# Performance work log

Hardware: AMD Instinct MI355X
Metric: run time of the kernel (lower is better)

## Reference

```python
import jax, jax.numpy as jnp
import numpy as np

H = 512
IN_DIM = 300
NUM_CLASSES = 45
LN_EPS = 1e-5


def _ln(x, g, b):
    m = jnp.mean(x, axis=-1, keepdims=True)
    v = jnp.mean((x - m) ** 2, axis=-1, keepdims=True)
    return (x - m) / jnp.sqrt(v + LN_EPS) * g + b


def _rnn_dir(xemb, Wx, bx, Wh, bh, ln_g, ln_b):
    # xemb: [B, T, H]; Wx/Wh: [3, H, H]; bx/bh: [3, H]; ln_g/ln_b: [3, H]
    B = xemb.shape[0]
    h_init = (jnp.zeros((B, H), xemb.dtype),) * 3

    def step(carry, xt):
        h0, h1, h2 = carry
        h0 = jnp.tanh(_ln(xt @ Wx[0] + bx[0] + h0 @ Wh[0] + bh[0], ln_g[0], ln_b[0]))
        h1 = jnp.tanh(_ln(h0 @ Wx[1] + bx[1] + h1 @ Wh[1] + bh[1], ln_g[1], ln_b[1]))
        h2 = jnp.tanh(_ln(h1 @ Wx[2] + bx[2] + h2 @ Wh[2] + bh[2], ln_g[2], ln_b[2]))
        return (h0, h1, h2), h2

    _, ys = jax.lax.scan(step, h_init, jnp.swapaxes(xemb, 0, 1))  # ys: [T, B, H]
    return jnp.swapaxes(ys, 0, 1)  # [B, T, H]


def setup_inputs() -> dict:
    key = jax.random.key(0)
    ks = jax.random.split(key, 20)
    B, T = 128, 256
    s_in = 1.0 / np.sqrt(IN_DIM)
    s_h = 1.0 / np.sqrt(H)
    inp = {
        "x": jax.random.normal(ks[0], (B, T, IN_DIM), jnp.float32),
        "reverse_x": jax.random.normal(ks[1], (B, T, IN_DIM), jnp.float32),
        "pad_start_index": jax.random.randint(ks[2], (B,), 0, T),
        "max_length": T,
        "W_emb": jax.random.uniform(ks[3], (IN_DIM, H), jnp.float32, -s_in, s_in),
        "b_emb": jax.random.uniform(ks[4], (H,), jnp.float32, -s_in, s_in),
        "Wx_l2r": jax.random.uniform(ks[5], (3, H, H), jnp.float32, -s_h, s_h),
        "bx_l2r": jax.random.uniform(ks[6], (3, H), jnp.float32, -s_h, s_h),
        "Wh_l2r": jax.random.uniform(ks[7], (3, H, H), jnp.float32, -s_h, s_h),
        "bh_l2r": jax.random.uniform(ks[8], (3, H), jnp.float32, -s_h, s_h),
        "Wx_r2l": jax.random.uniform(ks[9], (3, H, H), jnp.float32, -s_h, s_h),
        "bx_r2l": jax.random.uniform(ks[10], (3, H), jnp.float32, -s_h, s_h),
        "Wh_r2l": jax.random.uniform(ks[11], (3, H, H), jnp.float32, -s_h, s_h),
        "bh_r2l": jax.random.uniform(ks[12], (3, H), jnp.float32, -s_h, s_h),
        "ln_g": jnp.ones((3, H), jnp.float32),
        "ln_b": jnp.zeros((3, H), jnp.float32),
        "W_fc": jax.random.uniform(ks[13], (2 * H, NUM_CLASSES), jnp.float32, -1.0 / np.sqrt(2 * H), 1.0 / np.sqrt(2 * H)),
        "b_fc": jax.random.uniform(ks[14], (NUM_CLASSES,), jnp.float32, -1.0 / np.sqrt(2 * H), 1.0 / np.sqrt(2 * H)),
    }
    return inp


def reference(x, reverse_x, pad_start_index, max_length, W_emb, b_emb,
              Wx_l2r, bx_l2r, Wh_l2r, bh_l2r, Wx_r2l, bx_r2l, Wh_r2l, bh_r2l,
              ln_g, ln_b, W_fc, b_fc):
    x = x[:, :max_length]
    reverse_x = reverse_x[:, :max_length]
    x_l2r = x @ W_emb + b_emb           # [B, T, H]
    x_r2l = reverse_x @ W_emb + b_emb
    out_l2r = _rnn_dir(x_l2r, Wx_l2r, bx_l2r, Wh_l2r, bh_l2r, ln_g, ln_b)
    out_r2l = _rnn_dir(x_r2l, Wx_r2l, bx_r2l, Wh_r2l, bh_r2l, ln_g, ln_b)
    T = out_l2r.shape[1]
    j = jnp.arange(T)[None, :]
    p = pad_start_index[:, None]
    idx = jnp.where(j < p, p - j - 1, j)  # [B, T] gather index into r2l time axis
    r2l_g = jnp.take_along_axis(out_r2l, idx[:, :, None], axis=1)
    concat = jnp.concatenate([out_l2r, r2l_g], axis=-1)  # [B, T, 2H]
    logit = concat @ W_fc + b_fc
    return logit.reshape(-1, logit.shape[-1])
```

## Files before the change

kernel.cpp:

```cpp
#include <hip/hip_runtime.h>

#define Bdim 128
#define Tdim 256
#define Hdim 512
#define INdim 300
#define KXdim 320
#define NC 45
#define NTHR 256
#define FPAD 16

typedef _Float16 h16;
typedef __attribute__((ext_vector_type(8))) _Float16 half8;
typedef __attribute__((ext_vector_type(4))) float float4v;
typedef __attribute__((ext_vector_type(2))) float float2v;
typedef __attribute__((ext_vector_type(4))) uint uint4v;
typedef unsigned long long u64;

__device__ __forceinline__ int ld_flag(const int* p) {
    return __hip_atomic_load((int*)p, __ATOMIC_RELAXED, __HIP_MEMORY_SCOPE_AGENT);
}
__device__ __forceinline__ void st_flag_rel(int* p, int v) {
    __hip_atomic_store(p, v, __ATOMIC_RELEASE, __HIP_MEMORY_SCOPE_AGENT);
}

#define WAIT_VM() do { \
    asm volatile("s_waitcnt vmcnt(0)" ::: "memory"); \
    __builtin_amdgcn_sched_barrier(0); \
} while (0)

__device__ __forceinline__ half8 ld16v(const h16* p) {
    half8 r;
    asm volatile("global_load_dwordx4 %0, %1, off sc0 sc1"
                 : "=&v"(r) : "v"(p) : "memory");
    return r;
}
__device__ __forceinline__ float2v ld8vf(const float* p) {
    float2v r;
    asm volatile("global_load_dwordx2 %0, %1, off sc0 sc1"
                 : "=&v"(r) : "v"(p) : "memory");
    return r;
}
__device__ __forceinline__ void st16v(h16* p, half8 v) {
    asm volatile("global_store_dwordx4 %0, %1, off sc0 sc1"
                 :: "v"(p), "v"(v) : "memory");
}
__device__ __forceinline__ void st16vf(float* p, uint4v v) {
    asm volatile("global_store_dwordx4 %0, %1, off sc0 sc1"
                 :: "v"(p), "v"(v) : "memory");
}

__global__ __launch_bounds__(NTHR) void prep1_kernel(
    const float* Wemb, const float* bemb,
    const float* Wx_l2r, const float* bx_l2r, const float* bh_l2r,
    const float* Wx_r2l, const float* bx_r2l, const float* bh_r2l,
    float* W0, float* cb)
{
    int gid = blockIdx.x * NTHR + threadIdx.x;
    const int nW0 = 2 * KXdim * Hdim;
    if (gid < nW0) {
        int dir = gid / (KXdim * Hdim);
        int rem = gid % (KXdim * Hdim);
        int i = rem / Hdim, h = rem % Hdim;
        const float* Wx = dir ? Wx_r2l : Wx_l2r;
        float s = 0.f;
        if (i < INdim) {
            for (int k = 0; k < Hdim; ++k)
                s += Wemb[i * Hdim + k] * Wx[k * Hdim + h];
        }
        W0[gid] = s;
    } else {
        int idx = gid - nW0;
        if (idx < 2 * 3 * Hdim) {
            int dir = idx / (3 * Hdim);
            int l = (idx / Hdim) % 3;
            int h = idx % Hdim;
            const float* Wx = dir ? Wx_r2l : Wx_l2r;
            const float* bx = dir ? bx_r2l : bx_l2r;
            const float* bh = dir ? bh_r2l : bh_l2r;
            float s = bx[l * Hdim + h] + bh[l * Hdim + h];
            if (l == 0) {
                for (int k = 0; k < Hdim; ++k)
                    s += bemb[k] * Wx[k * Hdim + h];
            }
            cb[idx] = s;
        }
    }
}

__global__ __launch_bounds__(NTHR) void pack_W_kernel(
    const float* W0,
    const float* Wx_l2r, const float* Wh_l2r,
    const float* Wx_r2l, const float* Wh_r2l,
    h16* Wfrag)
{
    int e = blockIdx.x * NTHR + threadIdx.x;
    if (e >= 6 * 16 * 32 * 2 * 64 * 8) return;
    int j    = e & 7;
    int lane = (e >> 3) & 63;
    int nt   = (e >> 9) & 1;
    int ks   = (e >> 10) & 31;
    int cs   = (e >> 15) & 15;
    int u    = e >> 19;
    int dir = u / 3, l = u % 3;
    int n  = cs * 32 + nt * 16 + (lane & 15);
    int kk = ks * 32 + ((lane >> 4) * 8) + j;
    float v;
    if (kk < 512) {
        if (l == 0) {
            v = (kk < KXdim) ? W0[(dir * KXdim + kk) * Hdim + n] : 0.f;
        } else {
            const float* Wx = dir ? Wx_r2l : Wx_l2r;
            v = Wx[(l * Hdim + kk) * Hdim + n];
        }
    } else {
        const float* Wh = dir ? Wh_r2l : Wh_l2r;
        v = Wh[(l * Hdim + (kk - 512)) * Hdim + n];
    }
    Wfrag[e] = (h16)v;
}

__global__ __launch_bounds__(NTHR) void pack_W0f_kernel(const float* W0, h16* W0f)
{
    int e = blockIdx.x * NTHR + threadIdx.x;
    if (e >= 2 * 32 * 10 * 64 * 8) return;
    int j    = e & 7;
    int lane = (e >> 3) & 63;
    int rest = e >> 9;
    int ks   = rest % 10;
    rest /= 10;
    int nt   = rest & 31;
    int dir  = rest >> 5;
    int k = ks * 32 + ((lane >> 4) * 8) + j;
    int n = nt * 16 + (lane & 15);
    W0f[e] = (h16)W0[(dir * KXdim + k) * Hdim + n];
}

__global__ __launch_bounds__(NTHR) void zx0_kernel(
    const float* __restrict__ x0, const float* __restrict__ x1,
    const h16* __restrict__ W0f, const float* __restrict__ cb,
    h16* __restrict__ zx0f)
{
    int bx = blockIdx.x;
    int t = bx & 255, mh = (bx >> 8) & 1, dir = bx >> 9;
    const int tid = threadIdx.x;
    __shared__ h16 xl[64 * 328];
    const float* xs = dir ? x1 : x0;
    for (int i = tid; i < 64 * 328; i += NTHR) {
        int r = i / 328, k = i - r * 328;
        int b = mh * 64 + r;
        float v = (k < INdim) ? xs[(b * Tdim + t) * INdim + k] : 0.f;
        xl[i] = (h16)v;
    }
    __syncthreads();
    int wave = tid >> 6, lane = tid & 63;
    int r15 = lane & 15, q = lane >> 4;
    for (int nt = 0; nt < 32; ++nt) {
        float4v acc = {0.f, 0.f, 0.f, 0.f};
        #pragma unroll
        for (int ks = 0; ks < 10; ++ks) {
            half8 af = *(const half8*)&xl[(wave * 16 + r15) * 328 + ks * 32 + q * 8];
            half8 bf = *(const half8*)&W0f[(((dir * 32 + nt) * 10 + ks) * 64 + lane) * 8];
            acc = __builtin_amdgcn_mfma_f32_16x16x32_f16(af, bf, acc, 0, 0, 0);
        }
        int col = nt * 16 + r15;
        float cbv = cb[(dir * 3 + 0) * Hdim + col];
        union { h16 h[4]; uint2 u2; } o;
        #pragma unroll
        for (int r = 0; r < 4; ++r) o.h[r] = (h16)(acc[r] + cbv);
        h16* dst = zx0f + (((( (size_t)dir * Tdim + t) * 32 + nt) * 8 + (mh * 4 + wave)) * 64 + lane) * 4;
        *(uint2*)dst = o.u2;
    }
}

__global__ __launch_bounds__(NTHR) void zeroinit_kernel(int* hdone, int* sdone)
{
    int gid = blockIdx.x * NTHR + threadIdx.x;
    if (gid < 192 * FPAD) { hdone[gid] = 0; sdone[gid] = 0; }
}

struct PipeArgs {
    const h16* Wfrag;
    const h16* zx0f;
    const float* cb;
    const float* lng;
    const float* lnb;
    h16* hbuf;
    float* pstat;
    h16* h2;
    int* hdone;
    int* sdone;
};

__device__ __forceinline__ size_t hb_idx(int u, int slot, int rh, int kf, int mt) {
    return ((((size_t)(u * 4 + slot) * 2 + rh) * 16 + kf) * 4 + mt) * 512;
}

__global__ __launch_bounds__(NTHR, 2) void rnn_pipe(PipeArgs a)
{
    const int blk = blockIdx.x, tid = threadIdx.x;
    const int w = tid >> 6, lane = tid & 63;
    const int r15 = lane & 15, quad = lane >> 4;
    const int u = blk >> 5, rh = (blk >> 4) & 1, cs = blk & 15;
    const int dir = u / 3, l = u % 3;

    __shared__ h16 wlds[32768];
    __shared__ h16 tile[4][512];
    __shared__ float mr[64][2];

    {
        const h16* wsrc = a.Wfrag + (size_t)(u * 16 + cs) * 32768;
        for (int i = tid * 8; i < 32768; i += NTHR * 8)
            *(uint4*)&wlds[i] = *(const uint4*)&wsrc[i];
    }
    float g2[2], b2[2], cbv[2];
    #pragma unroll
    for (int n = 0; n < 2; ++n) {
        int col = cs * 32 + n * 16 + r15;
        g2[n] = 2.0f * a.lng[l * Hdim + col];
        b2[n] = 2.0f * a.lnb[l * Hdim + col];
        cbv[n] = (l > 0) ? a.cb[(dir * 3 + l) * Hdim + col] : 0.f;
    }
    __syncthreads();

    const int fl = ((u * 2 + rh) * 16 + cs) * FPAD;
    const int gmt = rh * 4 + w;

    for (int t = 0; t < Tdim; ++t) {
        for (;;) {
            int ok = 1;
            if (tid < 16) {
                if (t > 0) ok = (ld_flag(&a.hdone[((u * 2 + rh) * 16 + tid) * FPAD]) >= t);
            } else if (tid >= 64 && tid < 80) {
                if (l > 0) ok = (ld_flag(&a.hdone[(((u - 1) * 2 + rh) * 16 + (tid - 64)) * FPAD]) >= t + 1);
            } else if (tid >= 128 && tid < 144) {
                if (l < 2 && t >= 4) ok = (ld_flag(&a.hdone[(((u + 1) * 2 + rh) * 16 + (tid - 128)) * FPAD]) >= t - 3);
            }
            if (__syncthreads_and(ok)) break;
            __builtin_amdgcn_s_sleep(1);
        }
        asm volatile("" ::: "memory");

        float4v acc0, acc1;
        if (l == 0) {
            const h16* zp = a.zx0f +
                ((((size_t)dir * Tdim + t) * 32 + cs * 2) * 8 + gmt) * 256 + lane * 4;
            union { uint2 uu; h16 hh[4]; } v0, v1;
            v0.uu = *(const uint2*)zp;
            v1.uu = *(const uint2*)(zp + 2048);
            #pragma unroll
            for (int r = 0; r < 4; ++r) { acc0[r] = (float)v0.hh[r]; acc1[r] = (float)v1.hh[r]; }
        } else {
            acc0 = (float4v){0.f, 0.f, 0.f, 0.f};
            acc1 = (float4v){0.f, 0.f, 0.f, 0.f};
        }

        half8 afL[16], afP[16];
        if (l > 0) {
            const h16* hbL = a.hbuf + hb_idx(u - 1, t & 3, rh, 0, w) + lane * 8;
            #pragma unroll
            for (int ks = 0; ks < 16; ++ks)
                afL[ks] = ld16v(hbL + (size_t)ks * 2048);
        }
        if (t > 0) {
            const h16* hbP = a.hbuf + hb_idx(u, (t + 3) & 3, rh, 0, w) + lane * 8;
            #pragma unroll
            for (int ks = 0; ks < 16; ++ks)
                afP[ks] = ld16v(hbP + (size_t)ks * 2048);
        }
        WAIT_VM();
        if (l > 0) {
            #pragma unroll
            for (int ks = 0; ks < 16; ++ks) {
                half8 b0 = *(const half8*)&wlds[((ks * 2 + 0) * 64 + lane) * 8];
                half8 b1 = *(const half8*)&wlds[((ks * 2 + 1) * 64 + lane) * 8];
                acc0 = __builtin_amdgcn_mfma_f32_16x16x32_f16(afL[ks], b0, acc0, 0, 0, 0);
                acc1 = __builtin_amdgcn_mfma_f32_16x16x32_f16(afL[ks], b1, acc1, 0, 0, 0);
            }
        }
        if (t > 0) {
            #pragma unroll
            for (int ks = 0; ks < 16; ++ks) {
                half8 b0 = *(const half8*)&wlds[(((ks + 16) * 2 + 0) * 64 + lane) * 8];
                half8 b1 = *(const half8*)&wlds[(((ks + 16) * 2 + 1) * 64 + lane) * 8];
                acc0 = __builtin_amdgcn_mfma_f32_16x16x32_f16(afP[ks], b0, acc0, 0, 0, 0);
                acc1 = __builtin_amdgcn_mfma_f32_16x16x32_f16(afP[ks], b1, acc1, 0, 0, 0);
            }
        }
        #pragma unroll
        for (int r = 0; r < 4; ++r) { acc0[r] += cbv[0]; acc1[r] += cbv[1]; }

        {
            float sr[4], qr[4];
            #pragma unroll
            for (int r = 0; r < 4; ++r) {
                float s = acc0[r] + acc1[r];
                float q = __builtin_fmaf(acc0[r], acc0[r], acc1[r] * acc1[r]);
                s += __shfl_xor(s, 1); q += __shfl_xor(q, 1);
                s += __shfl_xor(s, 2); q += __shfl_xor(q, 2);
                s += __shfl_xor(s, 4); q += __shfl_xor(q, 4);
                s += __shfl_xor(s, 8); q += __shfl_xor(q, 8);
                sr[r] = s; qr[r] = q;
            }
            if (r15 == 0) {
                float* pb = a.pstat + ((((size_t)(u * 4 + (t & 3)) * 2 + rh) * 16 + cs) * 64) * 2
                          + (w * 16 + quad * 4) * 2;
                union { float f[4]; uint4v u; } v1, v2;
                v1.f[0] = sr[0]; v1.f[1] = qr[0]; v1.f[2] = sr[1]; v1.f[3] = qr[1];
                v2.f[0] = sr[2]; v2.f[1] = qr[2]; v2.f[2] = sr[3]; v2.f[3] = qr[3];
                st16vf(pb, v1.u);
                st16vf(pb + 4, v2.u);
            }
        }
        asm volatile("s_waitcnt vmcnt(0)" ::: "memory");
        __syncthreads();
        if (tid == 0) st_flag_rel(&a.sdone[fl], t + 1);

        for (;;) {
            int ok = 1;
            if (tid < 16) ok = (ld_flag(&a.sdone[((u * 2 + rh) * 16 + tid) * FPAD]) >= t + 1);
            if (__syncthreads_and(ok)) break;
            __builtin_amdgcn_s_sleep(1);
        }
        asm volatile("" ::: "memory");

        if (tid < 64) {
            const float* pb = a.pstat + (((size_t)(u * 4 + (t & 3)) * 2 + rh) * 16) * 128;
            float2v pv[16];
            #pragma unroll
            for (int c = 0; c < 16; ++c)
                pv[c] = ld8vf(pb + (c * 64 + tid) * 2);
            WAIT_VM();
            float ss = 0.f, qq = 0.f;
            #pragma unroll
            for (int c = 0; c < 16; ++c) { ss += pv[c][0]; qq += pv[c][1]; }
            float m = ss * (1.0f / Hdim);
            float var = qq * (1.0f / Hdim) - m * m;
            float rstd = rsqrtf(var + 1e-5f);
            mr[tid][0] = rstd;
            mr[tid][1] = -m * rstd;
        }
        __syncthreads();

        #pragma unroll
        for (int r = 0; r < 4; ++r) {
            int row = quad * 4 + r;
            int grow = w * 16 + row;
            float A = mr[grow][0], C = mr[grow][1];
            float x0 = __builtin_fmaf(__builtin_fmaf(acc0[r], A, C), g2[0], b2[0]);
            float x1 = __builtin_fmaf(__builtin_fmaf(acc1[r], A, C), g2[1], b2[1]);
            float E0 = __expf(x0), E1 = __expf(x1);
            int sw = (row >> 2) << 3;
            tile[w][row * 32 + ((r15) ^ sw)]      = (h16)(1.0f - __fdividef(2.0f, E0 + 1.0f));
            tile[w][row * 32 + ((16 + r15) ^ sw)] = (h16)(1.0f - __fdividef(2.0f, E1 + 1.0f));
        }
        {
            int row = lane & 15;
            int cb2 = (quad * 8) ^ ((row >> 2) << 3);
            half8 v = *(const half8*)&tile[w][row * 32 + cb2];
            st16v(a.hbuf + hb_idx(u, t & 3, rh, cs, w) + lane * 8, v);
        }
        if (l == 2) {
            int row = lane >> 2, cg = (lane & 3) * 8;
            uint4 v = *(const uint4*)&tile[w][row * 32 + (cg ^ ((row >> 2) << 3))];
            int grow = rh * 64 + w * 16 + row;
            *(uint4*)&a.h2[(((size_t)dir * Tdim + t) * Bdim + grow) * Hdim + cs * 32 + cg] = v;
        }
        asm volatile("s_waitcnt vmcnt(0)" ::: "memory");
        __syncthreads();
        if (tid == 0) st_flag_rel(&a.hdone[fl], t + 1);
    }
}

__global__ __launch_bounds__(NTHR) void fc_kernel(
    const h16* __restrict__ h2, const int* __restrict__ pad,
    const float* __restrict__ Wfc, const float* __restrict__ bfc,
    float* __restrict__ out)
{
    __shared__ float sA[64 * 68];
    __shared__ float sB[64 * 48];
    const int blk = blockIdx.x, tid = threadIdx.x;
    const int b = blk >> 2;
    const int j0 = (blk & 3) * 64;
    const int p = pad[b];
    const int rg = tid >> 4;
    const int c0 = (tid & 15) * 3;
    float acc[4][3] = {};

    for (int k0 = 0; k0 < 2 * Hdim; k0 += 64) {
        {
            int rr = tid >> 2;
            int kp = (tid & 3) * 16;
            int j = j0 + rr;
            const h16* src;
            if (k0 < Hdim) {
                src = h2 + (((size_t)0 * Tdim + j) * Bdim + b) * Hdim + k0 + kp;
            } else {
                int idx = (j < p) ? (p - j - 1) : j;
                src = h2 + (((size_t)1 * Tdim + idx) * Bdim + b) * Hdim + (k0 - Hdim) + kp;
            }
            union { uint4 u4; h16 h[8]; } w0, w1;
            w0.u4 = *(const uint4*)src;
            w1.u4 = *(const uint4*)(src + 8);
            #pragma unroll
            for (int i = 0; i < 8; ++i) {
                sA[rr * 68 + kp + i]     = (float)w0.h[i];
                sA[rr * 68 + kp + 8 + i] = (float)w1.h[i];
            }
        }
        for (int e = tid; e < 64 * 48; e += NTHR) {
            int kk = e / 48, c = e - kk * 48;
            sB[e] = (c < NC) ? Wfc[(k0 + kk) * NC + c] : 0.f;
        }
        __syncthreads();
        for (int kk = 0; kk < 64; ++kk) {
            float b0 = sB[kk * 48 + c0 + 0];
            float b1 = sB[kk * 48 + c0 + 1];
            float b2 = sB[kk * 48 + c0 + 2];
            #pragma unroll
            for (int i = 0; i < 4; ++i) {
                float av = sA[(rg * 4 + i) * 68 + kk];
                acc[i][0] += av * b0; acc[i][1] += av * b1; acc[i][2] += av * b2;
            }
        }
        __syncthreads();
    }
    #pragma unroll
    for (int i = 0; i < 4; ++i) {
        int r = blk * 64 + rg * 4 + i;
        #pragma unroll
        for (int jj = 0; jj < 3; ++jj) {
            int c = c0 + jj;
            if (c < NC) out[r * NC + c] = acc[i][jj] + bfc[c];
        }
    }
}

extern "C" void kernel_launch(void* const* d_in, const int* in_sizes, int n_in,
                              void* d_out, int out_size, void* d_ws, size_t ws_size,
                              hipStream_t stream) {
    const float* x      = (const float*)d_in[0];
    const float* rx     = (const float*)d_in[1];
    const int*   pad    = (const int*)d_in[2];
    const float* Wemb   = (const float*)d_in[4];
    const float* bemb   = (const float*)d_in[5];
    const float* Wx_l2r = (const float*)d_in[6];
    const float* bx_l2r = (const float*)d_in[7];
    const float* Wh_l2r = (const float*)d_in[8];
    const float* bh_l2r = (const float*)d_in[9];
    const float* Wx_r2l = (const float*)d_in[10];
    const float* bx_r2l = (const float*)d_in[11];
    const float* Wh_r2l = (const float*)d_in[12];
    const float* bh_r2l = (const float*)d_in[13];
    const float* lng    = (const float*)d_in[14];
    const float* lnb    = (const float*)d_in[15];
    const float* Wfc    = (const float*)d_in[16];
    const float* bfc    = (const float*)d_in[17];

    char* base = (char*)d_ws;
    size_t off = 0;
    auto alloc = [&](size_t bytes) { char* p = base + off; off += (bytes + 255) & ~(size_t)255; return p; };
    h16*   zx0f  = (h16*)  alloc((size_t)2 * Tdim * 32 * 8 * 64 * 4 * 2);
    h16*   h2    = (h16*)  alloc((size_t)2 * Tdim * Bdim * Hdim * 2);
    h16*   Wfrag = (h16*)  alloc((size_t)6 * 16 * 32768 * 2);
    h16*   W0f   = (h16*)  alloc((size_t)2 * 32 * 10 * 64 * 8 * 2);
    h16*   hbuf  = (h16*)  alloc((size_t)6 * 4 * 2 * 16 * 4 * 512 * 2);
    float* pstat = (float*)alloc((size_t)6 * 4 * 2 * 16 * 64 * 2 * 4);
    float* W0    = (float*)alloc((size_t)2 * KXdim * Hdim * 4);
    float* cb    = (float*)alloc((size_t)2 * 3 * Hdim * 4);
    int*   hdone = (int*)  alloc((size_t)192 * FPAD * 4);
    int*   sdone = (int*)  alloc((size_t)192 * FPAD * 4);

    prep1_kernel<<<(2 * KXdim * Hdim + 2 * 3 * Hdim) / NTHR, NTHR, 0, stream>>>(
        Wemb, bemb, Wx_l2r, bx_l2r, bh_l2r, Wx_r2l, bx_r2l, bh_r2l, W0, cb);

    pack_W_kernel<<<(6 * 16 * 32 * 2 * 64 * 8) / NTHR, NTHR, 0, stream>>>(
        W0, Wx_l2r, Wh_l2r, Wx_r2l, Wh_r2l, Wfrag);

    pack_W0f_kernel<<<(2 * 32 * 10 * 64 * 8) / NTHR, NTHR, 0, stream>>>(W0, W0f);

    zx0_kernel<<<1024, NTHR, 0, stream>>>(x, rx, W0f, cb, zx0f);

    zeroinit_kernel<<<(192 * FPAD + NTHR - 1) / NTHR, NTHR, 0, stream>>>(hdone, sdone);

    PipeArgs a;
    a.Wfrag = Wfrag; a.zx0f = zx0f; a.cb = cb; a.lng = lng; a.lnb = lnb;
    a.hbuf = hbuf; a.pstat = pstat; a.h2 = h2;
    a.hdone = hdone; a.sdone = sdone;
    void* kargs[] = { &a };
    hipLaunchCooperativeKernel((void*)rnn_pipe, dim3(192), dim3(NTHR), kargs, 0, stream);

    fc_kernel<<<(Bdim * Tdim) / 64, NTHR, 0, stream>>>(h2, pad, Wfc, bfc, (float*)d_out);
}
```

Baseline: 3.734 ms.

## Pack sync flags densely and poll them from a single wavefront

```diff
diff --git a/kernel.cpp b/kernel.cpp
--- a/kernel.cpp
+++ b/kernel.cpp
@@ -7,7 +7,6 @@
 #define KXdim 320
 #define NC 45
 #define NTHR 256
-#define FPAD 16
 
 typedef _Float16 h16;
 typedef __attribute__((ext_vector_type(8))) _Float16 half8;
@@ -172,10 +171,10 @@
     }
 }
 
-__global__ __launch_bounds__(NTHR) void zeroinit_kernel(int* hdone, int* sdone)
+__global__ __launch_bounds__(NTHR) void zeroinit_kernel(int* hflag, int* sflag)
 {
     int gid = blockIdx.x * NTHR + threadIdx.x;
-    if (gid < 192 * FPAD) { hdone[gid] = 0; sdone[gid] = 0; }
+    if (gid < 12 * 16) { hflag[gid] = 0; sflag[gid] = 0; }
 }
 
 struct PipeArgs {
@@ -187,8 +186,8 @@
     h16* hbuf;
     float* pstat;
     h16* h2;
-    int* hdone;
-    int* sdone;
+    int* hflag;
+    int* sflag;
 };
 
 __device__ __forceinline__ size_t hb_idx(int u, int slot, int rh, int kf, int mt) {
@@ -202,6 +201,7 @@
     const int r15 = lane & 15, quad = lane >> 4;
     const int u = blk >> 5, rh = (blk >> 4) & 1, cs = blk & 15;
     const int dir = u / 3, l = u % 3;
+    const int g = u * 2 + rh;
 
     __shared__ h16 wlds[32768];
     __shared__ h16 tile[4][512];
@@ -222,22 +222,30 @@
     }
     __syncthreads();
 
-    const int fl = ((u * 2 + rh) * 16 + cs) * FPAD;
     const int gmt = rh * 4 + w;
 
+    const int* w1p = nullptr;
+    int w1role = 0;
+    if (w == 0) {
+        if (lane < 16)      { w1p = &a.hflag[g * 16 + lane];        w1role = 1; }
+        else if (lane < 32) { if (l > 0) { w1p = &a.hflag[(g - 2) * 16 + (lane - 16)]; w1role = 2; } }
+        else if (lane < 48) { if (l < 2) { w1p = &a.hflag[(g + 2) * 16 + (lane - 32)]; w1role = 3; } }
+    }
+
     for (int t = 0; t < Tdim; ++t) {
-        for (;;) {
-            int ok = 1;
-            if (tid < 16) {
-                if (t > 0) ok = (ld_flag(&a.hdone[((u * 2 + rh) * 16 + tid) * FPAD]) >= t);
-            } else if (tid >= 64 && tid < 80) {
-                if (l > 0) ok = (ld_flag(&a.hdone[(((u - 1) * 2 + rh) * 16 + (tid - 64)) * FPAD]) >= t + 1);
-            } else if (tid >= 128 && tid < 144) {
-                if (l < 2 && t >= 4) ok = (ld_flag(&a.hdone[(((u + 1) * 2 + rh) * 16 + (tid - 128)) * FPAD]) >= t - 3);
-            }
-            if (__syncthreads_and(ok)) break;
-            __builtin_amdgcn_s_sleep(1);
-        }
+        if (w == 0) {
+            int tgt = 0, act = 0;
+            if (w1role == 1) { tgt = t;     act = (t > 0); }
+            if (w1role == 2) { tgt = t + 1; act = 1; }
+            if (w1role == 3) { tgt = t - 3; act = (t >= 4); }
+            for (;;) {
+                int ok = 1;
+                if (act) ok = (ld_flag(w1p) >= tgt);
+                if (__all(ok)) break;
+                __builtin_amdgcn_s_sleep(2);
+            }
+        }
+        __syncthreads();
         asm volatile("" ::: "memory");
 
         float4v acc0, acc1;
@@ -313,14 +321,17 @@
         }
         asm volatile("s_waitcnt vmcnt(0)" ::: "memory");
         __syncthreads();
-        if (tid == 0) st_flag_rel(&a.sdone[fl], t + 1);
-
-        for (;;) {
-            int ok = 1;
-            if (tid < 16) ok = (ld_flag(&a.sdone[((u * 2 + rh) * 16 + tid) * FPAD]) >= t + 1);
-            if (__syncthreads_and(ok)) break;
-            __builtin_amdgcn_s_sleep(1);
-        }
+        if (tid == 0) st_flag_rel(&a.sflag[g * 16 + cs], t + 1);
+
+        if (w == 0) {
+            const int* sp = &a.sflag[g * 16 + (lane & 15)];
+            for (;;) {
+                int ok = (lane < 16) ? (ld_flag(sp) >= t + 1) : 1;
+                if (__all(ok)) break;
+                __builtin_amdgcn_s_sleep(2);
+            }
+        }
+        __syncthreads();
         asm volatile("" ::: "memory");
 
         if (tid < 64) {
@@ -367,7 +378,7 @@
         }
         asm volatile("s_waitcnt vmcnt(0)" ::: "memory");
         __syncthreads();
-        if (tid == 0) st_flag_rel(&a.hdone[fl], t + 1);
+        if (tid == 0) st_flag_rel(&a.hflag[g * 16 + cs], t + 1);
     }
 }
 
@@ -467,8 +478,8 @@
     float* pstat = (float*)alloc((size_t)6 * 4 * 2 * 16 * 64 * 2 * 4);
     float* W0    = (float*)alloc((size_t)2 * KXdim * Hdim * 4);
     float* cb    = (float*)alloc((size_t)2 * 3 * Hdim * 4);
-    int*   hdone = (int*)  alloc((size_t)192 * FPAD * 4);
-    int*   sdone = (int*)  alloc((size_t)192 * FPAD * 4);
+    int*   hflag = (int*)  alloc((size_t)12 * 16 * 4);
+    int*   sflag = (int*)  alloc((size_t)12 * 16 * 4);
 
     prep1_kernel<<<(2 * KXdim * Hdim + 2 * 3 * Hdim) / NTHR, NTHR, 0, stream>>>(
         Wemb, bemb, Wx_l2r, bx_l2r, bh_l2r, Wx_r2l, bx_r2l, bh_r2l, W0, cb);
@@ -480,12 +491,12 @@
 
     zx0_kernel<<<1024, NTHR, 0, stream>>>(x, rx, W0f, cb, zx0f);
 
-    zeroinit_kernel<<<(192 * FPAD + NTHR - 1) / NTHR, NTHR, 0, stream>>>(hdone, sdone);
+    zeroinit_kernel<<<1, NTHR, 0, stream>>>(hflag, sflag);
 
     PipeArgs a;
     a.Wfrag = Wfrag; a.zx0f = zx0f; a.cb = cb; a.lng = lng; a.lnb = lnb;
     a.hbuf = hbuf; a.pstat = pstat; a.h2 = h2;
-    a.hdone = hdone; a.sdone = sdone;
+    a.hflag = hflag; a.sflag = sflag;
     void* kargs[] = { &a };
     hipLaunchCooperativeKernel((void*)rnn_pipe, dim3(192), dim3(NTHR), kargs, 0, stream);
 
```

Result: no change. 3.763 ms (+0.8%).
